# Kernel optimization log

Measured on AMD Instinct MI355X. Metric: run time of the kernel, lower is better.

The kernel has to match this reference:

```python
import jax, jax.numpy as jnp
import numpy as np

_SUBPIXEL_EPS = 1e-6


def spiral_pattern(sz_y: int, sz_x: int) -> np.ndarray:
    pattern = np.zeros((2 * sz_y + 1, 2 * sz_x + 1), dtype=np.float32)
    radius = sz_y
    n = 0
    for dy in range(radius + 1):
        for direction in range(4):
            dx_start = -dy
            limit = 1 if direction == 0 and dy == 0 else dy
            for dx in range(dx_start, limit):
                if direction == 0:
                    wx_b, wy_b = radius + dx, radius + dy
                elif direction == 1:
                    wx_b, wy_b = radius + dy, radius - dx
                elif direction == 2:
                    wx_b, wy_b = radius - dx, radius - dy
                else:
                    wx_b, wy_b = radius - dy, radius + dx
                n += 1
                pattern[wy_b, wx_b] = n
    return pattern


def argmin_centered_spiral(x, sz):
    # x: [..., num_ch] float32 cost values; spiral tie-break, no cv_offset.
    num_ch = (2 * sz + 1) ** 2
    min_val = jnp.min(x, axis=-1, keepdims=True)
    default_mask = (x == min_val).astype(jnp.float32)
    central_bias = jnp.asarray(spiral_pattern(sz, sz).reshape(num_ch)) * _SUBPIXEL_EPS
    central = default_mask - central_bias
    mask = (central == jnp.max(central, axis=-1, keepdims=True)).astype(jnp.float32)
    ch_range = jnp.arange(num_ch, dtype=jnp.float32)
    final = mask - ch_range * _SUBPIXEL_EPS
    one_hot = (final == jnp.max(final, axis=-1, keepdims=True)).astype(jnp.float32)
    return jnp.sum(one_hot * ch_range, axis=-1).astype(jnp.int32)


def setup_inputs() -> dict:
    key = jax.random.key(0)
    k1, k2 = jax.random.split(key)
    B, H, W, K = 1, 135, 240, 16
    sr = 4
    C = (2 * sr + 1) ** 2 + 1  # 81 block-match candidates + 1 input-MV channel
    windows = jax.random.randint(k1, (B, H, W, C, K), 0, 256).astype(jnp.float32)
    templates = jax.random.randint(k2, (B, H, W, 1, K), 0, 256).astype(jnp.float32)
    return {"windows": windows, "templates": templates, "search_range": sr}


def reference(windows, templates, search_range):
    B, H, W, C, K = windows.shape
    sr = int(search_range)
    # SAD cost volume (inputs are integer-valued; float32 sums are exact here)
    cost = jnp.sum(jnp.abs(windows - templates), axis=-1)  # [B,H,W,C]
    input_mv_idx = (2 * sr + 1) ** 2
    # motion-vector LUT
    rng = jnp.arange(-sr, sr + 1, dtype=jnp.float32)
    jj, ii = jnp.meshgrid(rng, rng, indexing="ij")
    vec_lut = (-1.0 * jnp.stack([jj, ii], axis=-1).reshape(-1, 2)).astype(jnp.float16)
    # spiral-tie-break argmin over block-match candidates
    idx_bm = argmin_centered_spiral(cost[..., :input_mv_idx], sr)[..., None]  # [B,H,W,1]
    min_cost_bm = jnp.take_along_axis(cost, idx_bm, axis=3)  # [B,H,W,1]
    has_input_mv = (C - 1) == input_mv_idx
    if has_input_mv:
        cost_at_input_mv = cost[..., -1:]
        input_mv_mask = cost_at_input_mv < min_cost_bm
        min_idx = jnp.where(input_mv_mask, input_mv_idx, idx_bm)
        min_cost_volume = jnp.minimum(cost_at_input_mv, min_cost_bm)
    else:
        input_mv_mask = jnp.zeros_like(min_cost_bm, dtype=bool)
        min_idx = idx_bm
        min_cost_volume = min_cost_bm
    vector = vec_lut[idx_bm[..., 0]]  # [B,H,W,2]
    min_templates = jnp.take_along_axis(windows, min_idx[..., None], axis=3)  # [B,H,W,1,K]
    return (vector, min_templates, input_mv_mask, min_cost_volume.astype(jnp.int32))
```

## Files before the change

### kernel.cpp

```cpp
#include <hip/hip_runtime.h>

#define KDIM 16
#define NSPIRAL 81

typedef float f4 __attribute__((ext_vector_type(4)));

__device__ __constant__ int d_spiral[NSPIRAL] = {
 74,73,72,71,70,69,68,67,66,
 75,44,43,42,41,40,39,38,65,
 76,45,22,21,20,19,18,37,64,
 77,46,23, 8, 7, 6,17,36,63,
 78,47,24, 9, 1, 5,16,35,62,
 79,48,25, 2, 3, 4,15,34,61,
 80,49,10,11,12,13,14,33,60,
 81,26,27,28,29,30,31,32,59,
 50,51,52,53,54,55,56,57,58
};

template<int C_CONST>
__global__ __launch_bounds__(256) void calc_vector_kernel(
    const float* __restrict__ windows,
    const float* __restrict__ templates,
    float* __restrict__ out,
    int npix, int C_rt)
{
    __shared__ int s_spiral[NSPIRAL];
    const int tid = threadIdx.x;
    if (tid < NSPIRAL) s_spiral[tid] = d_spiral[tid];
    __syncthreads();

    const int C   = (C_CONST > 0) ? C_CONST : C_rt;
    const int wave = tid >> 6;
    const int lane = tid & 63;
    const int pix = blockIdx.x * 4 + wave;
    if (pix >= npix) return;

    const int rowlen = C * KDIM;
    const int nf4 = rowlen >> 2;
    const float* wrow = windows + (size_t)pix * rowlen;

    const int kseg = (lane & 3) * 4;
    const f4 t4 = __builtin_nontemporal_load(
        reinterpret_cast<const f4*>(templates + (size_t)pix * KDIM + kseg));

    int bestkey = 0x7FFFFFFF;
    int cost81 = 0;

    #pragma unroll
    for (int it = 0; it < 6; ++it) {
        const int f = it * 64 + lane;
        const int c = it * 16 + (lane >> 2);
        const bool active = (C_CONST > 0) ? (it < (nf4 >> 6) || (f < nf4))
                                          : (f < nf4);
        float s = 0.0f;
        if (active) {
            const f4 w4 = __builtin_nontemporal_load(
                reinterpret_cast<const f4*>(wrow + f * 4));
            s = fabsf(w4.x - t4.x) + fabsf(w4.y - t4.y) +
                fabsf(w4.z - t4.z) + fabsf(w4.w - t4.w);
        }
        s += __shfl_xor(s, 1);
        s += __shfl_xor(s, 2);
        const int cost = (int)s;
        if (active && c < NSPIRAL) {
            const int n = s_spiral[c];
            const int key = (cost << 14) | (n << 7) | c;
            bestkey = min(bestkey, key);
        }
        if (active && c == NSPIRAL) cost81 = cost;
    }

    #pragma unroll
    for (int off = 32; off >= 1; off >>= 1)
        bestkey = min(bestkey, __shfl_xor(bestkey, off));
    cost81 = __shfl(cost81, 4);

    const int idx_bm      = bestkey & 127;
    const int min_cost_bm = bestkey >> 14;
    const bool mv_mask    = cost81 < min_cost_bm;
    const int min_idx     = mv_mask ? NSPIRAL : idx_bm;
    const int mcv         = min(cost81, min_cost_bm);

    float* out_vec  = out;
    float* out_tmpl = out + (size_t)npix * 2;
    float* out_mask = out + (size_t)npix * 18;
    float* out_cost = out + (size_t)npix * 19;

    if (lane < 4) {
        const f4 w4 = *reinterpret_cast<const f4*>(wrow + min_idx * KDIM + lane * 4);
        __builtin_nontemporal_store(w4,
            reinterpret_cast<f4*>(out_tmpl + (size_t)pix * KDIM + lane * 4));
    }
    if (lane == 0) {
        out_vec[(size_t)pix * 2 + 0] = (float)(4 - idx_bm / 9);
        out_vec[(size_t)pix * 2 + 1] = (float)(4 - idx_bm % 9);
        out_mask[pix] = mv_mask ? 1.0f : 0.0f;
        out_cost[pix] = (float)mcv;
    }
}

extern "C" void kernel_launch(void* const* d_in, const int* in_sizes, int n_in,
                              void* d_out, int out_size, void* d_ws, size_t ws_size,
                              hipStream_t stream) {
    const float* windows   = (const float*)d_in[0];
    const float* templates = (const float*)d_in[1];
    float* out = (float*)d_out;

    const int npix = in_sizes[1] / KDIM;
    const int C    = in_sizes[0] / in_sizes[1];

    const int blocks = (npix + 3) / 4;
    if (C == 82) {
        calc_vector_kernel<82><<<blocks, 256, 0, stream>>>(windows, templates, out, npix, C);
    } else {
        calc_vector_kernel<-1><<<blocks, 256, 0, stream>>>(windows, templates, out, npix, C);
    }
}
```

Measured before the change: 32.39 us.

## Process two pixels per wave and gather winning template from registers

Each wavefront now handles two pixels, issuing all window loads for both up front to raise memory-level parallelism and halve block count. The selected template row is taken from the already-loaded registers via cross-lane shuffles instead of re-reading global memory. Small outputs are written as vectorised f4/f2 stores for the pixel pair. This raises register pressure (12 f4 per lane), which may reduce occupancy.

```diff
diff --git a/kernel.cpp b/kernel.cpp
--- a/kernel.cpp
+++ b/kernel.cpp
@@ -4,6 +4,7 @@
 #define NSPIRAL 81
 
 typedef float f4 __attribute__((ext_vector_type(4)));
+typedef float f2 __attribute__((ext_vector_type(2)));
 
 __device__ __constant__ int d_spiral[NSPIRAL] = {
  74,73,72,71,70,69,68,67,66,
@@ -29,73 +30,127 @@
     if (tid < NSPIRAL) s_spiral[tid] = d_spiral[tid];
     __syncthreads();
 
-    const int C   = (C_CONST > 0) ? C_CONST : C_rt;
+    const int C    = (C_CONST > 0) ? C_CONST : C_rt;
     const int wave = tid >> 6;
     const int lane = tid & 63;
-    const int pix = blockIdx.x * 4 + wave;
-    if (pix >= npix) return;
+    const int wgid = blockIdx.x * 4 + wave;
+    const int pix0 = wgid * 2;
+    const int pix1 = pix0 + 1;
+    if (pix0 >= npix) return;
+    const bool has1 = (pix1 < npix);
 
     const int rowlen = C * KDIM;
     const int nf4 = rowlen >> 2;
-    const float* wrow = windows + (size_t)pix * rowlen;
+    const float* wrow0 = windows + (size_t)pix0 * rowlen;
+    const float* wrow1 = windows + (size_t)pix1 * rowlen;
 
     const int kseg = (lane & 3) * 4;
-    const f4 t4 = __builtin_nontemporal_load(
-        reinterpret_cast<const f4*>(templates + (size_t)pix * KDIM + kseg));
+    const f4 tA = __builtin_nontemporal_load(
+        reinterpret_cast<const f4*>(templates + (size_t)pix0 * KDIM + kseg));
+    f4 tB = tA;
+    if (has1) tB = __builtin_nontemporal_load(
+        reinterpret_cast<const f4*>(templates + (size_t)pix1 * KDIM + kseg));
 
-    int bestkey = 0x7FFFFFFF;
-    int cost81 = 0;
+    f4 a[6], b[6];
+    #pragma unroll
+    for (int it = 0; it < 6; ++it) {
+        const int f = it * 64 + lane;
+        const bool act = f < ((C_CONST > 0) ? (C_CONST * 4) : nf4);
+        a[it] = f4{0.f, 0.f, 0.f, 0.f};
+        b[it] = f4{0.f, 0.f, 0.f, 0.f};
+        if (act) a[it] = __builtin_nontemporal_load(
+            reinterpret_cast<const f4*>(wrow0 + f * 4));
+        if (act && has1) b[it] = __builtin_nontemporal_load(
+            reinterpret_cast<const f4*>(wrow1 + f * 4));
+    }
 
+    int bk0 = 0x7FFFFFFF, bk1 = 0x7FFFFFFF;
+    int c810 = 0, c811 = 0;
     #pragma unroll
     for (int it = 0; it < 6; ++it) {
         const int f = it * 64 + lane;
         const int c = it * 16 + (lane >> 2);
-        const bool active = (C_CONST > 0) ? (it < (nf4 >> 6) || (f < nf4))
-                                          : (f < nf4);
-        float s = 0.0f;
-        if (active) {
-            const f4 w4 = __builtin_nontemporal_load(
-                reinterpret_cast<const f4*>(wrow + f * 4));
-            s = fabsf(w4.x - t4.x) + fabsf(w4.y - t4.y) +
-                fabsf(w4.z - t4.z) + fabsf(w4.w - t4.w);
+        const bool act = f < ((C_CONST > 0) ? (C_CONST * 4) : nf4);
+        float s0 = fabsf(a[it].x - tA.x) + fabsf(a[it].y - tA.y) +
+                   fabsf(a[it].z - tA.z) + fabsf(a[it].w - tA.w);
+        float s1 = fabsf(b[it].x - tB.x) + fabsf(b[it].y - tB.y) +
+                   fabsf(b[it].z - tB.z) + fabsf(b[it].w - tB.w);
+        s0 += __shfl_xor(s0, 1);  s1 += __shfl_xor(s1, 1);
+        s0 += __shfl_xor(s0, 2);  s1 += __shfl_xor(s1, 2);
+        if (act && c < NSPIRAL) {
+            const int nb = (s_spiral[c] << 7) | c;
+            bk0 = min(bk0, ((int)s0 << 14) | nb);
+            bk1 = min(bk1, ((int)s1 << 14) | nb);
         }
-        s += __shfl_xor(s, 1);
-        s += __shfl_xor(s, 2);
-        const int cost = (int)s;
-        if (active && c < NSPIRAL) {
-            const int n = s_spiral[c];
-            const int key = (cost << 14) | (n << 7) | c;
-            bestkey = min(bestkey, key);
-        }
-        if (active && c == NSPIRAL) cost81 = cost;
+        if (act && c == NSPIRAL) { c810 = (int)s0; c811 = (int)s1; }
     }
 
     #pragma unroll
-    for (int off = 32; off >= 1; off >>= 1)
-        bestkey = min(bestkey, __shfl_xor(bestkey, off));
-    cost81 = __shfl(cost81, 4);
+    for (int off = 32; off >= 1; off >>= 1) {
+        bk0 = min(bk0, __shfl_xor(bk0, off));
+        bk1 = min(bk1, __shfl_xor(bk1, off));
+    }
+    c810 = __shfl(c810, 4);
+    c811 = __shfl(c811, 4);
 
-    const int idx_bm      = bestkey & 127;
-    const int min_cost_bm = bestkey >> 14;
-    const bool mv_mask    = cost81 < min_cost_bm;
-    const int min_idx     = mv_mask ? NSPIRAL : idx_bm;
-    const int mcv         = min(cost81, min_cost_bm);
+    const int idx0 = bk0 & 127, mc0 = bk0 >> 14;
+    const bool m0  = c810 < mc0;
+    const int mi0  = m0 ? NSPIRAL : idx0;
+    const int mcv0 = min(c810, mc0);
+    const int idx1 = bk1 & 127, mc1 = bk1 >> 14;
+    const bool m1  = c811 < mc1;
+    const int mi1  = m1 ? NSPIRAL : idx1;
+    const int mcv1 = min(c811, mc1);
+
+    f4 sel0, sel1;
+    switch (mi0 >> 4) {
+        case 0: sel0 = a[0]; break;  case 1: sel0 = a[1]; break;
+        case 2: sel0 = a[2]; break;  case 3: sel0 = a[3]; break;
+        case 4: sel0 = a[4]; break;  default: sel0 = a[5]; break;
+    }
+    switch (mi1 >> 4) {
+        case 0: sel1 = b[0]; break;  case 1: sel1 = b[1]; break;
+        case 2: sel1 = b[2]; break;  case 3: sel1 = b[3]; break;
+        case 4: sel1 = b[4]; break;  default: sel1 = b[5]; break;
+    }
+    const int sl0 = (mi0 & 15) * 4 + (lane & 3);
+    const int sl1 = (mi1 & 15) * 4 + (lane & 3);
+    f4 win0, win1;
+    win0.x = __shfl(sel0.x, sl0); win0.y = __shfl(sel0.y, sl0);
+    win0.z = __shfl(sel0.z, sl0); win0.w = __shfl(sel0.w, sl0);
+    win1.x = __shfl(sel1.x, sl1); win1.y = __shfl(sel1.y, sl1);
+    win1.z = __shfl(sel1.z, sl1); win1.w = __shfl(sel1.w, sl1);
 
     float* out_vec  = out;
     float* out_tmpl = out + (size_t)npix * 2;
     float* out_mask = out + (size_t)npix * 18;
     float* out_cost = out + (size_t)npix * 19;
 
-    if (lane < 4) {
-        const f4 w4 = *reinterpret_cast<const f4*>(wrow + min_idx * KDIM + lane * 4);
-        __builtin_nontemporal_store(w4,
-            reinterpret_cast<f4*>(out_tmpl + (size_t)pix * KDIM + lane * 4));
+    if (lane < 8 && (lane < 4 || has1)) {
+        const int  p = (lane < 4) ? pix0 : pix1;
+        const f4   w = (lane < 4) ? win0 : win1;
+        __builtin_nontemporal_store(w,
+            reinterpret_cast<f4*>(out_tmpl + (size_t)p * KDIM + (lane & 3) * 4));
     }
     if (lane == 0) {
-        out_vec[(size_t)pix * 2 + 0] = (float)(4 - idx_bm / 9);
-        out_vec[(size_t)pix * 2 + 1] = (float)(4 - idx_bm % 9);
-        out_mask[pix] = mv_mask ? 1.0f : 0.0f;
-        out_cost[pix] = (float)mcv;
+        if (has1) {
+            f4 v; v.x = (float)(4 - idx0 / 9); v.y = (float)(4 - idx0 % 9);
+                  v.z = (float)(4 - idx1 / 9); v.w = (float)(4 - idx1 % 9);
+            __builtin_nontemporal_store(v,
+                reinterpret_cast<f4*>(out_vec + (size_t)pix0 * 2));
+            f2 mm; mm.x = m0 ? 1.f : 0.f; mm.y = m1 ? 1.f : 0.f;
+            __builtin_nontemporal_store(mm,
+                reinterpret_cast<f2*>(out_mask + pix0));
+            f2 cc; cc.x = (float)mcv0; cc.y = (float)mcv1;
+            __builtin_nontemporal_store(cc,
+                reinterpret_cast<f2*>(out_cost + pix0));
+        } else {
+            f2 v; v.x = (float)(4 - idx0 / 9); v.y = (float)(4 - idx0 % 9);
+            __builtin_nontemporal_store(v,
+                reinterpret_cast<f2*>(out_vec + (size_t)pix0 * 2));
+            out_mask[pix0] = m0 ? 1.f : 0.f;
+            out_cost[pix0] = (float)mcv0;
+        }
     }
 }
 
@@ -109,7 +164,8 @@
     const int npix = in_sizes[1] / KDIM;
     const int C    = in_sizes[0] / in_sizes[1];
 
-    const int blocks = (npix + 3) / 4;
+    const int npair  = (npix + 1) / 2;
+    const int blocks = (npair + 3) / 4;
     if (C == 82) {
         calc_vector_kernel<82><<<blocks, 256, 0, stream>>>(windows, templates, out, npix, C);
     } else {
```

Result: slower. 33.69 us (+4.0%).
